# Kernel optimization log

Hardware: AMD Instinct MI355X
Metric: run time of the kernel (lower is better)

Reference implementation:

```python
import jax, jax.numpy as jnp
import numpy as np

ENT_SIZE = 100000; REL_SIZE = 500; ENT_DIM = 256; REL_DIM = 256; H = 256
E = 2048; S = 32; N = 1024; THRESHOLD = 1.0; EPS = 1e-5


def _xav(k, shape):
    fan_in = shape[-1]
    fan_out = shape[-2] if len(shape) > 1 else shape[-1]
    std = (2.0 / (fan_in + fan_out)) ** 0.5
    return jax.random.normal(k, shape, jnp.float32) * std


def setup_inputs() -> dict:
    key = jax.random.key(0)
    ks = jax.random.split(key, 16)
    inp = {}
    inp["neighbors"] = jax.random.randint(ks[0], (E, S), 0, ENT_SIZE)
    inp["pos_h"] = jax.random.randint(ks[1], (N,), 0, E)
    inp["pos_t"] = jax.random.randint(ks[2], (N,), 0, E)
    inp["pos_r"] = jax.random.randint(ks[3], (N,), 0, REL_SIZE)
    inp["neg_h"] = jax.random.randint(ks[4], (N,), 0, E)
    inp["neg_t"] = jax.random.randint(ks[5], (N,), 0, E)
    inp["neg_r"] = jax.random.randint(ks[6], (N,), 0, REL_SIZE)
    inp["ent_embed"] = _xav(ks[7], (ENT_SIZE + 1, ENT_DIM))
    inp["rel_embed"] = _xav(ks[8], (REL_SIZE, REL_DIM))
    inp["trans"] = _xav(ks[9], (2 * REL_SIZE, REL_DIM, ENT_DIM))
    inp["W_ih_f"] = _xav(ks[10], (4 * H, ENT_DIM)); inp["W_hh_f"] = _xav(ks[11], (4 * H, H))
    inp["W_ih_b"] = _xav(ks[12], (4 * H, ENT_DIM)); inp["W_hh_b"] = _xav(ks[13], (4 * H, H))
    inp["b_f"] = jnp.zeros((4 * H,), jnp.float32)
    inp["b_b"] = jnp.zeros((4 * H,), jnp.float32)
    inp["W_lin"] = _xav(ks[14], (ENT_DIM, 2 * H)); inp["b_lin"] = jnp.zeros((ENT_DIM,), jnp.float32)
    inp["gamma"] = jnp.ones((ENT_DIM,), jnp.float32); inp["beta"] = jnp.zeros((ENT_DIM,), jnp.float32)
    return inp


def _lstm_final(x, W_ih, W_hh, b):
    # x: [E,S,D] -> final hidden state [E,H] (PyTorch LSTM gate order i,f,g,o; b = b_ih+b_hh)
    h0 = jnp.zeros((x.shape[0], H), x.dtype)
    def step(carry, xt):
        h, c = carry
        g = xt @ W_ih.T + h @ W_hh.T + b  # [E,4H]
        i, f, gg, o = jnp.split(g, 4, axis=-1)
        c = jax.nn.sigmoid(f) * c + jax.nn.sigmoid(i) * jnp.tanh(gg)
        h = jax.nn.sigmoid(o) * jnp.tanh(c)
        return (h, c), None
    (h, _), _ = jax.lax.scan(step, (h0, h0), jnp.swapaxes(x, 0, 1))
    return h


def _context(ent_embed, neighbors, W_ih_f, W_hh_f, b_f, W_ih_b, W_hh_b, b_b, W_lin, b_lin, gamma, beta):
    x_seq = ent_embed[neighbors]  # [E,S,D]
    h_f = _lstm_final(x_seq, W_ih_f, W_hh_f, b_f)
    h_b = _lstm_final(x_seq[:, ::-1], W_ih_b, W_hh_b, b_b)
    lin = jnp.concatenate([h_f, h_b], -1) @ W_lin.T + b_lin  # [E,ENT_DIM]
    # BatchNorm1d in training mode: batch stats (biased variance)
    mu = lin.mean(0)
    var = lin.var(0)
    return jnp.tanh(gamma * (lin - mu) * jax.lax.rsqrt(var + EPS) + beta)


def _score(trans, rel_embed, ctx, h_idx, r_idx, t_idx):
    Wh = trans[r_idx]             # [N,REL_DIM,ENT_DIM] (grouped expert GEMV, batched)
    Wt = trans[r_idx + REL_SIZE]
    d = jnp.einsum('nre,ne->nr', Wh, ctx[h_idx]) - jnp.einsum('nre,ne->nr', Wt, ctx[t_idx])
    return jnp.linalg.norm(d + rel_embed[r_idx], axis=1)


def reference(neighbors, pos_h, pos_t, pos_r, neg_h, neg_t, neg_r,
              ent_embed, rel_embed, trans, W_ih_f, W_hh_f, W_ih_b, W_hh_b,
              b_f, b_b, W_lin, b_lin, gamma, beta):
    ctx = _context(ent_embed, neighbors, W_ih_f, W_hh_f, b_f, W_ih_b, W_hh_b, b_b,
                   W_lin, b_lin, gamma, beta)
    pos_n = _score(trans, rel_embed, ctx, pos_h, pos_r, pos_t)
    neg_n = _score(trans, rel_embed, ctx, neg_h, neg_r, neg_t)
    return jnp.sum(pos_n + jax.nn.relu(THRESHOLD - neg_n))
```

## Files before the change

### kernel.cpp

```cpp
#include <hip/hip_runtime.h>

constexpr int kE   = 2048;
constexpr int kS   = 32;
constexpr int kD   = 256;
constexpr int kG4  = 1024;
constexpr int kK   = 512;
constexpr int kREL = 500;
constexpr int kN   = 1024;

typedef unsigned short u16;
typedef __attribute__((ext_vector_type(8))) _Float16 f16x8;
typedef __attribute__((ext_vector_type(4))) float    f32x4;

static __device__ __forceinline__ u16 f2h(float f) {
  _Float16 h = (_Float16)f;
  return __builtin_bit_cast(u16, h);
}

__global__ void prep_weights(const float* __restrict__ Wih_f, const float* __restrict__ Whh_f,
                             const float* __restrict__ Wih_b, const float* __restrict__ Whh_b,
                             const float* __restrict__ Wlin_in,
                             u16* __restrict__ Wcat_f, u16* __restrict__ Wcat_b,
                             u16* __restrict__ Wlin) {
  int idx = blockIdx.x * 256 + threadIdx.x;
  if (idx < kG4 * kK) {
    int n = idx >> 9, k = idx & 511;
    float vf = (k < 256) ? Wih_f[n * 256 + k] : Whh_f[n * 256 + (k - 256)];
    float vb = (k < 256) ? Wih_b[n * 256 + k] : Whh_b[n * 256 + (k - 256)];
    Wcat_f[idx] = f2h(vf);
    Wcat_b[idx] = f2h(vb);
  }
  if (idx < 256 * kK) Wlin[idx] = f2h(Wlin_in[idx]);
}

__global__ void gather_x(const int* __restrict__ neighbors, const float* __restrict__ ent,
                         u16* __restrict__ x16) {
  const int tot = kS * kE * kD / 4;
  for (int i = blockIdx.x * blockDim.x + threadIdx.x; i < tot; i += gridDim.x * blockDim.x) {
    int k4 = i & 63;
    int row = i >> 6;
    int e = row & (kE - 1);
    int t = row >> 11;
    int nb = neighbors[e * kS + t];
    float4 v = *(const float4*)(ent + (size_t)nb * kD + k4 * 4);
    ushort4 o;
    o.x = f2h(v.x); o.y = f2h(v.y); o.z = f2h(v.z); o.w = f2h(v.w);
    *(ushort4*)(x16 + (size_t)row * kD + k4 * 4) = o;
  }
}

template <bool GMAP>
static __device__ __forceinline__ void gemm_tile(
    const u16* __restrict__ Alo, const u16* __restrict__ Ahi,
    const u16* __restrict__ W, int e0, int u0,
    u16* As, u16* Bs, f32x4 (&acc)[4][4]) {
  const int tid = threadIdx.x;
  const int lane = tid & 63;
  const int w = tid >> 6;
#pragma unroll
  for (int m = 0; m < 4; m++)
#pragma unroll
    for (int n = 0; n < 4; n++) acc[m][n] = (f32x4){0.f, 0.f, 0.f, 0.f};

  for (int ch = 0; ch < 8; ++ch) {
    const int k0 = ch * 64;
    __syncthreads();
    const u16* Asrc = (k0 < 256) ? Alo : Ahi;
    const int kbase = (k0 < 256) ? k0 : (k0 - 256);
#pragma unroll
    for (int i = 0; i < 2; i++) {
      int idx = tid + i * 256;
      int row = idx >> 3, c8 = idx & 7;
      uint4 v = *(const uint4*)(Asrc + (size_t)(e0 + row) * 256 + kbase + c8 * 8);
      *(uint4*)((char*)As + row * 128 + ((c8 * 16) ^ ((row & 7) << 4))) = v;
    }
#pragma unroll
    for (int i = 0; i < 8; i++) {
      int idx = tid + i * 256;
      int j = idx >> 3, c8 = idx & 7;
      int n = GMAP ? ((j >> 6) * 256 + u0 + (j & 63)) : j;
      uint4 v = *(const uint4*)(W + (size_t)n * kK + k0 + c8 * 8);
      *(uint4*)((char*)Bs + j * 128 + ((c8 * 16) ^ ((j & 7) << 4))) = v;
    }
    __syncthreads();
#pragma unroll
    for (int ks = 0; ks < 2; ++ks) {
      const int kb = ks * 64 + (lane >> 4) * 16;
      f16x8 a[4], b[4];
#pragma unroll
      for (int m = 0; m < 4; m++) {
        int row = m * 16 + (lane & 15);
        a[m] = *(const f16x8*)((const char*)As + row * 128 + (kb ^ ((row & 7) << 4)));
      }
#pragma unroll
      for (int n = 0; n < 4; n++) {
        int row = w * 64 + n * 16 + (lane & 15);
        b[n] = *(const f16x8*)((const char*)Bs + row * 128 + (kb ^ ((row & 7) << 4)));
      }
#pragma unroll
      for (int m = 0; m < 4; m++)
#pragma unroll
        for (int n = 0; n < 4; n++)
          acc[m][n] = __builtin_amdgcn_mfma_f32_16x16x32_f16(a[m], b[n], acc[m][n], 0, 0, 0);
    }
  }
}

__global__ __launch_bounds__(256) void lstm_step(
    const u16* __restrict__ x16, const u16* __restrict__ Wcat_f, const u16* __restrict__ Wcat_b,
    const float* __restrict__ b_f, const float* __restrict__ b_b,
    const u16* __restrict__ hprev, u16* __restrict__ hnext,
    float* __restrict__ cbuf, int t) {
  __shared__ __align__(16) char smem[65536];
  u16* As = (u16*)smem;
  u16* Bs = (u16*)(smem + 8192);
  float* Gs = (float*)smem;

  const int tid = threadIdx.x, lane = tid & 63, w = tid >> 6;
  const int e0 = blockIdx.x * 64, u0 = blockIdx.y * 64, dir = blockIdx.z;

  const u16* Wd = dir ? Wcat_b : Wcat_f;
  const float* bd = dir ? b_b : b_f;
  const u16* xsrc = x16 + (size_t)(dir ? (kS - 1 - t) : t) * kE * kD;
  const u16* hp = hprev + (size_t)dir * kE * kD;
  u16* hn = hnext + (size_t)dir * kE * kD;
  float* cd = cbuf + (size_t)dir * kE * kD;

  f32x4 acc[4][4];
  gemm_tile<true>(xsrc, hp, Wd, e0, u0, As, Bs, acc);

  __syncthreads();
#pragma unroll
  for (int m = 0; m < 4; m++)
#pragma unroll
    for (int n = 0; n < 4; n++)
#pragma unroll
      for (int r = 0; r < 4; r++)
        Gs[(m * 16 + (lane >> 4) * 4 + r) * 256 + w * 64 + n * 16 + (lane & 15)] = acc[m][n][r];
  __syncthreads();

#pragma unroll
  for (int i = 0; i < 16; i++) {
    int cell = tid + i * 256;
    int er = cell >> 6, uu = cell & 63;
    float gi = Gs[er * 256 + uu]        + bd[u0 + uu];
    float gf = Gs[er * 256 + 64 + uu]   + bd[256 + u0 + uu];
    float gg = Gs[er * 256 + 128 + uu]  + bd[512 + u0 + uu];
    float go = Gs[er * 256 + 192 + uu]  + bd[768 + u0 + uu];
    size_t off = (size_t)(e0 + er) * kD + u0 + uu;
    float c_old = cd[off];
    float si = 1.f / (1.f + __expf(-gi));
    float sf = 1.f / (1.f + __expf(-gf));
    float so = 1.f / (1.f + __expf(-go));
    float cn = sf * c_old + si * tanhf(gg);
    cd[off] = cn;
    hn[off] = f2h(so * tanhf(cn));
  }
}

__global__ __launch_bounds__(256) void lin_kernel(
    const u16* __restrict__ hf, const u16* __restrict__ hb,
    const u16* __restrict__ Wl, const float* __restrict__ b_lin,
    float* __restrict__ lin) {
  __shared__ __align__(16) char smem[40960];
  u16* As = (u16*)smem;
  u16* Bs = (u16*)(smem + 8192);
  const int tid = threadIdx.x, lane = tid & 63, w = tid >> 6;
  const int e0 = blockIdx.x * 64;
  f32x4 acc[4][4];
  gemm_tile<false>(hf, hb, Wl, e0, 0, As, Bs, acc);
#pragma unroll
  for (int m = 0; m < 4; m++)
#pragma unroll
    for (int n = 0; n < 4; n++)
#pragma unroll
      for (int r = 0; r < 4; r++) {
        int e = e0 + m * 16 + (lane >> 4) * 4 + r;
        int col = w * 64 + n * 16 + (lane & 15);
        lin[(size_t)e * 256 + col] = acc[m][n][r] + b_lin[col];
      }
}

__global__ void bn_stats(const float* __restrict__ lin, float* __restrict__ part) {
  int b = blockIdx.x, c = threadIdx.x;
  float s = 0.f, s2 = 0.f;
  for (int e = b * 256; e < b * 256 + 256; ++e) {
    float x = lin[(size_t)e * 256 + c];
    s += x; s2 += x * x;
  }
  part[b * 256 + c] = s;
  part[2048 + b * 256 + c] = s2;
}

__global__ void bn_finalize(const float* __restrict__ part, float* __restrict__ mus) {
  int c = threadIdx.x;
  float s = 0.f, s2 = 0.f;
  for (int b = 0; b < 8; b++) { s += part[b * 256 + c]; s2 += part[2048 + b * 256 + c]; }
  float mu = s * (1.f / 2048.f);
  float var = s2 * (1.f / 2048.f) - mu * mu;
  mus[c] = mu;
  mus[256 + c] = rsqrtf(var + 1e-5f);
}

__global__ void bn_tanh(const float* __restrict__ lin, const float* __restrict__ mus,
                        const float* __restrict__ gamma, const float* __restrict__ beta,
                        float* __restrict__ ctx) {
  int idx = blockIdx.x * 256 + threadIdx.x;
  int c = idx & 255;
  float x = lin[idx];
  ctx[idx] = tanhf(gamma[c] * (x - mus[c]) * mus[256 + c] + beta[c]);
}

__global__ __launch_bounds__(256) void score_kernel(
    const float* __restrict__ ctx, const float* __restrict__ trans,
    const float* __restrict__ rel_embed,
    const int* __restrict__ ph, const int* __restrict__ pt, const int* __restrict__ pr,
    const int* __restrict__ nh, const int* __restrict__ nt, const int* __restrict__ nr,
    float* __restrict__ scores) {
  int n = blockIdx.x;
  bool pos = n < kN;
  int m = n & (kN - 1);
  int hi = pos ? ph[m] : nh[m];
  int ti = pos ? pt[m] : nt[m];
  int ri = pos ? pr[m] : nr[m];
  __shared__ float ch[256], ct[256];
  __shared__ float wsum[4];
  int tid = threadIdx.x;
  ch[tid] = ctx[(size_t)hi * 256 + tid];
  ct[tid] = ctx[(size_t)ti * 256 + tid];
  __syncthreads();
  const float4* Wh = (const float4*)(trans + (size_t)ri * 65536 + (size_t)tid * 256);
  const float4* Wt = (const float4*)(trans + ((size_t)ri + kREL) * 65536 + (size_t)tid * 256);
  const float4* c4h = (const float4*)ch;
  const float4* c4t = (const float4*)ct;
  float acc = rel_embed[ri * 256 + tid];
#pragma unroll 4
  for (int q = 0; q < 64; q++) {
    float4 w1 = Wh[q], x1 = c4h[q];
    float4 w2 = Wt[q], x2 = c4t[q];
    acc += w1.x * x1.x + w1.y * x1.y + w1.z * x1.z + w1.w * x1.w;
    acc -= w2.x * x2.x + w2.y * x2.y + w2.z * x2.z + w2.w * x2.w;
  }
  float sq = acc * acc;
  for (int off = 32; off; off >>= 1) sq += __shfl_down(sq, off);
  if ((tid & 63) == 0) wsum[tid >> 6] = sq;
  __syncthreads();
  if (tid == 0) scores[n] = sqrtf(wsum[0] + wsum[1] + wsum[2] + wsum[3]);
}

__global__ void final_reduce(const float* __restrict__ scores, float* __restrict__ out) {
  int tid = threadIdx.x;
  float a = 0.f;
  for (int i = tid; i < 2 * kN; i += 256) {
    float s = scores[i];
    a += (i < kN) ? s : fmaxf(0.f, 1.f - s);
  }
  for (int off = 32; off; off >>= 1) a += __shfl_down(a, off);
  __shared__ float w4[4];
  if ((tid & 63) == 0) w4[tid >> 6] = a;
  __syncthreads();
  if (tid == 0) out[0] = w4[0] + w4[1] + w4[2] + w4[3];
}

extern "C" void kernel_launch(void* const* d_in, const int* in_sizes, int n_in,
                              void* d_out, int out_size, void* d_ws, size_t ws_size,
                              hipStream_t stream) {
  const int*   neighbors = (const int*)d_in[0];
  const int*   pos_h = (const int*)d_in[1];
  const int*   pos_t = (const int*)d_in[2];
  const int*   pos_r = (const int*)d_in[3];
  const int*   neg_h = (const int*)d_in[4];
  const int*   neg_t = (const int*)d_in[5];
  const int*   neg_r = (const int*)d_in[6];
  const float* ent_embed = (const float*)d_in[7];
  const float* rel_embed = (const float*)d_in[8];
  const float* trans = (const float*)d_in[9];
  const float* W_ih_f = (const float*)d_in[10];
  const float* W_hh_f = (const float*)d_in[11];
  const float* W_ih_b = (const float*)d_in[12];
  const float* W_hh_b = (const float*)d_in[13];
  const float* b_f = (const float*)d_in[14];
  const float* b_b = (const float*)d_in[15];
  const float* W_lin = (const float*)d_in[16];
  const float* b_lin = (const float*)d_in[17];
  const float* gamma = (const float*)d_in[18];
  const float* beta = (const float*)d_in[19];

  char* ws = (char*)d_ws;
  size_t off = 0;
  auto alloc = [&](size_t bytes) {
    void* p = ws + off;
    off = (off + bytes + 255) & ~(size_t)255;
    return p;
  };
  u16* Wcat_f = (u16*)alloc((size_t)kG4 * kK * 2);
  u16* Wcat_b = (u16*)alloc((size_t)kG4 * kK * 2);
  u16* Wlin   = (u16*)alloc((size_t)256 * kK * 2);
  u16* x16    = (u16*)alloc((size_t)kS * kE * kD * 2);
  u16* hbuf0  = (u16*)alloc((size_t)2 * kE * kD * 2);
  u16* hbuf1  = (u16*)alloc((size_t)2 * kE * kD * 2);
  float* cbuf = (float*)alloc((size_t)2 * kE * kD * 4);
  float* lin  = (float*)alloc((size_t)kE * 256 * 4);
  float* part = (float*)alloc((size_t)2 * 8 * 256 * 4);
  float* mus  = (float*)alloc((size_t)2 * 256 * 4);
  float* ctx  = (float*)alloc((size_t)kE * 256 * 4);
  float* scores = (float*)alloc((size_t)2 * kN * 4);
  (void)ws_size; (void)in_sizes; (void)n_in; (void)out_size;

  hipMemsetAsync(hbuf0, 0, (size_t)2 * kE * kD * 2, stream);
  hipMemsetAsync(cbuf, 0, (size_t)2 * kE * kD * 4, stream);

  prep_weights<<<2048, 256, 0, stream>>>(W_ih_f, W_hh_f, W_ih_b, W_hh_b, W_lin,
                                         Wcat_f, Wcat_b, Wlin);
  gather_x<<<4096, 256, 0, stream>>>(neighbors, ent_embed, x16);

  for (int t = 0; t < kS; ++t) {
    const u16* hp = (t & 1) ? hbuf1 : hbuf0;
    u16* hn = (t & 1) ? hbuf0 : hbuf1;
    lstm_step<<<dim3(32, 4, 2), 256, 0, stream>>>(x16, Wcat_f, Wcat_b, b_f, b_b, hp, hn, cbuf, t);
  }
  lin_kernel<<<dim3(32, 1), 256, 0, stream>>>(hbuf0, hbuf0 + (size_t)kE * kD, Wlin, b_lin, lin);
  bn_stats<<<8, 256, 0, stream>>>(lin, part);
  bn_finalize<<<1, 256, 0, stream>>>(part, mus);
  bn_tanh<<<2048, 256, 0, stream>>>(lin, mus, gamma, beta, ctx);
  score_kernel<<<2 * kN, 256, 0, stream>>>(ctx, trans, rel_embed,
                                           pos_h, pos_t, pos_r, neg_h, neg_t, neg_r, scores);
  final_reduce<<<1, 256, 0, stream>>>(scores, (float*)d_out);
}
```

Before: 860.2 us.

## Group score GEMVs by relation and use register-direct LSTM step with gate-interleaved weights

Weights are reordered so each wave's 16-column MFMA tiles hold the i,f,g,o gates for the same units. This lets the LSTM step apply the cell update straight from accumulators, with no LDS staging or extra barriers, and operands are loaded directly from global memory. Scoring now buckets triples by relation with a count/scan/scatter pass, so each relation's two 256x256 transform matrices are streamed once per group of up to 8 triples instead of once per triple. This cuts the dominant trans-matrix traffic, at the cost of several small extra kernel launches and load imbalance across relations. Fast exp-based tanh replaces tanhf.

```diff
diff --git a/kernel.cpp b/kernel.cpp
--- a/kernel.cpp
+++ b/kernel.cpp
@@ -16,19 +16,27 @@
   _Float16 h = (_Float16)f;
   return __builtin_bit_cast(u16, h);
 }
+static __device__ __forceinline__ float sigf(float x) { return 1.f / (1.f + __expf(-x)); }
+static __device__ __forceinline__ float tanhfast(float x) {
+  float e = __expf(2.f * x);
+  return 1.f - 2.f / (e + 1.f);
+}
 
 __global__ void prep_weights(const float* __restrict__ Wih_f, const float* __restrict__ Whh_f,
                              const float* __restrict__ Wih_b, const float* __restrict__ Whh_b,
                              const float* __restrict__ Wlin_in,
-                             u16* __restrict__ Wcat_f, u16* __restrict__ Wcat_b,
-                             u16* __restrict__ Wlin) {
+                             u16* __restrict__ Wr, u16* __restrict__ Wlin) {
   int idx = blockIdx.x * 256 + threadIdx.x;
   if (idx < kG4 * kK) {
-    int n = idx >> 9, k = idx & 511;
-    float vf = (k < 256) ? Wih_f[n * 256 + k] : Whh_f[n * 256 + (k - 256)];
-    float vb = (k < 256) ? Wih_b[n * 256 + k] : Whh_b[n * 256 + (k - 256)];
-    Wcat_f[idx] = f2h(vf);
-    Wcat_b[idx] = f2h(vb);
+    int rp = idx >> 9, k = idx & 511;
+    int g = (rp >> 4) & 3;
+    int u = (rp >> 6) * 16 + (rp & 15);
+    int row = g * 256 + u;
+    float vf, vb;
+    if (k < 256) { vf = Wih_f[row * 256 + k];        vb = Wih_b[row * 256 + k]; }
+    else         { vf = Whh_f[row * 256 + k - 256];  vb = Whh_b[row * 256 + k - 256]; }
+    Wr[idx] = f2h(vf);
+    Wr[kG4 * kK + idx] = f2h(vb);
   }
   if (idx < 256 * kK) Wlin[idx] = f2h(Wlin_in[idx]);
 }
@@ -49,6 +57,76 @@
   }
 }
 
+__global__ __launch_bounds__(256) void lstm_step_reg(
+    const u16* __restrict__ x16, const u16* __restrict__ Wr,
+    const float* __restrict__ b_f, const float* __restrict__ b_b,
+    const u16* __restrict__ hprev, u16* __restrict__ hnext,
+    float* __restrict__ cbuf, int t) {
+  const int tid = threadIdx.x, lane = tid & 63, w = tid >> 6;
+  const int bid = blockIdx.x;
+  const int dir = bid >> 7;
+  const int ut  = (bid >> 4) & 7;
+  const int et  = bid & 15;
+  const int wr = w >> 1, wc = w & 1;
+  const int e0 = et * 128 + wr * 64;
+  const int c0 = ut * 128 + wc * 64;
+  const int unit = (c0 >> 6) * 16 + (lane & 15);
+
+  const float* bd = dir ? b_b : b_f;
+  const u16* Wd  = Wr + (size_t)dir * kG4 * kK;
+  const u16* xs  = x16 + (size_t)(dir ? (kS - 1 - t) : t) * kE * kD;
+  const u16* hpd = hprev + (size_t)dir * kE * kD;
+  u16* hnd = hnext + (size_t)dir * kE * kD;
+  float* cd = cbuf + (size_t)dir * kE * kD;
+
+  const int klane = (lane >> 4) * 8;
+
+  f32x4 acc[4][4];
+#pragma unroll
+  for (int m = 0; m < 4; m++)
+#pragma unroll
+    for (int n = 0; n < 4; n++) acc[m][n] = (f32x4){0.f, 0.f, 0.f, 0.f};
+
+#pragma unroll
+  for (int ks = 0; ks < 16; ks++) {
+    const u16* asrc = (ks < 8) ? xs : hpd;
+    const int ka = (ks & 7) * 32 + klane;
+    f16x8 a[4], b[4];
+#pragma unroll
+    for (int m = 0; m < 4; m++) {
+      int row = e0 + m * 16 + (lane & 15);
+      a[m] = *(const f16x8*)(asrc + (size_t)row * kD + ka);
+    }
+#pragma unroll
+    for (int n = 0; n < 4; n++) {
+      int rowp = c0 + n * 16 + (lane & 15);
+      b[n] = *(const f16x8*)(Wd + (size_t)rowp * kK + ks * 32 + klane);
+    }
+#pragma unroll
+    for (int m = 0; m < 4; m++)
+#pragma unroll
+      for (int n = 0; n < 4; n++)
+        acc[m][n] = __builtin_amdgcn_mfma_f32_16x16x32_f16(a[m], b[n], acc[m][n], 0, 0, 0);
+  }
+
+  const float bi = bd[unit], bf_ = bd[256 + unit], bg = bd[512 + unit], bo = bd[768 + unit];
+#pragma unroll
+  for (int m = 0; m < 4; m++)
+#pragma unroll
+    for (int r = 0; r < 4; r++) {
+      int row = e0 + m * 16 + (lane >> 4) * 4 + r;
+      size_t off = (size_t)row * kD + unit;
+      float gi = acc[m][0][r] + bi;
+      float gf = acc[m][1][r] + bf_;
+      float gg = acc[m][2][r] + bg;
+      float go = acc[m][3][r] + bo;
+      float c_old = cd[off];
+      float cn = sigf(gf) * c_old + sigf(gi) * tanhfast(gg);
+      cd[off] = cn;
+      hnd[off] = f2h(sigf(go) * tanhfast(cn));
+    }
+}
+
 template <bool GMAP>
 static __device__ __forceinline__ void gemm_tile(
     const u16* __restrict__ Alo, const u16* __restrict__ Ahi,
@@ -103,58 +181,6 @@
         for (int n = 0; n < 4; n++)
           acc[m][n] = __builtin_amdgcn_mfma_f32_16x16x32_f16(a[m], b[n], acc[m][n], 0, 0, 0);
     }
-  }
-}
-
-__global__ __launch_bounds__(256) void lstm_step(
-    const u16* __restrict__ x16, const u16* __restrict__ Wcat_f, const u16* __restrict__ Wcat_b,
-    const float* __restrict__ b_f, const float* __restrict__ b_b,
-    const u16* __restrict__ hprev, u16* __restrict__ hnext,
-    float* __restrict__ cbuf, int t) {
-  __shared__ __align__(16) char smem[65536];
-  u16* As = (u16*)smem;
-  u16* Bs = (u16*)(smem + 8192);
-  float* Gs = (float*)smem;
-
-  const int tid = threadIdx.x, lane = tid & 63, w = tid >> 6;
-  const int e0 = blockIdx.x * 64, u0 = blockIdx.y * 64, dir = blockIdx.z;
-
-  const u16* Wd = dir ? Wcat_b : Wcat_f;
-  const float* bd = dir ? b_b : b_f;
-  const u16* xsrc = x16 + (size_t)(dir ? (kS - 1 - t) : t) * kE * kD;
-  const u16* hp = hprev + (size_t)dir * kE * kD;
-  u16* hn = hnext + (size_t)dir * kE * kD;
-  float* cd = cbuf + (size_t)dir * kE * kD;
-
-  f32x4 acc[4][4];
-  gemm_tile<true>(xsrc, hp, Wd, e0, u0, As, Bs, acc);
-
-  __syncthreads();
-#pragma unroll
-  for (int m = 0; m < 4; m++)
-#pragma unroll
-    for (int n = 0; n < 4; n++)
-#pragma unroll
-      for (int r = 0; r < 4; r++)
-        Gs[(m * 16 + (lane >> 4) * 4 + r) * 256 + w * 64 + n * 16 + (lane & 15)] = acc[m][n][r];
-  __syncthreads();
-
-#pragma unroll
-  for (int i = 0; i < 16; i++) {
-    int cell = tid + i * 256;
-    int er = cell >> 6, uu = cell & 63;
-    float gi = Gs[er * 256 + uu]        + bd[u0 + uu];
-    float gf = Gs[er * 256 + 64 + uu]   + bd[256 + u0 + uu];
-    float gg = Gs[er * 256 + 128 + uu]  + bd[512 + u0 + uu];
-    float go = Gs[er * 256 + 192 + uu]  + bd[768 + u0 + uu];
-    size_t off = (size_t)(e0 + er) * kD + u0 + uu;
-    float c_old = cd[off];
-    float si = 1.f / (1.f + __expf(-gi));
-    float sf = 1.f / (1.f + __expf(-gf));
-    float so = 1.f / (1.f + __expf(-go));
-    float cn = sf * c_old + si * tanhf(gg);
-    cd[off] = cn;
-    hn[off] = f2h(so * tanhf(cn));
   }
 }
 
@@ -211,41 +237,92 @@
   ctx[idx] = tanhf(gamma[c] * (x - mus[c]) * mus[256 + c] + beta[c]);
 }
 
-__global__ __launch_bounds__(256) void score_kernel(
+__global__ void count_rel(const int* __restrict__ pr, const int* __restrict__ nr,
+                          int* __restrict__ counts) {
+  int i = blockIdx.x * 256 + threadIdx.x;
+  if (i < kN) atomicAdd(&counts[pr[i]], 1);
+  else if (i < 2 * kN) atomicAdd(&counts[nr[i - kN]], 1);
+}
+
+__global__ void scan_rel(const int* __restrict__ counts, int* __restrict__ offs) {
+  __shared__ int s[512];
+  int tid = threadIdx.x;
+  s[tid] = (tid < kREL) ? counts[tid] : 0;
+  __syncthreads();
+  for (int d = 1; d < 512; d <<= 1) {
+    int v = (tid >= d) ? s[tid - d] : 0;
+    __syncthreads();
+    s[tid] += v;
+    __syncthreads();
+  }
+  if (tid == 0) offs[0] = 0;
+  if (tid <= kREL) offs[tid + 1] = s[tid];
+}
+
+__global__ void scatter_rel(const int* __restrict__ pr, const int* __restrict__ nr,
+                            const int* __restrict__ offs, int* __restrict__ cursor,
+                            int* __restrict__ list) {
+  int i = blockIdx.x * 256 + threadIdx.x;
+  if (i >= 2 * kN) return;
+  int r = (i < kN) ? pr[i] : nr[i - kN];
+  int p = atomicAdd(&cursor[r], 1);
+  list[offs[r] + p] = i;
+}
+
+__global__ __launch_bounds__(256) void score_grouped(
     const float* __restrict__ ctx, const float* __restrict__ trans,
     const float* __restrict__ rel_embed,
-    const int* __restrict__ ph, const int* __restrict__ pt, const int* __restrict__ pr,
-    const int* __restrict__ nh, const int* __restrict__ nt, const int* __restrict__ nr,
+    const int* __restrict__ ph, const int* __restrict__ pt,
+    const int* __restrict__ nh, const int* __restrict__ nt,
+    const int* __restrict__ offs, const int* __restrict__ list,
     float* __restrict__ scores) {
-  int n = blockIdx.x;
-  bool pos = n < kN;
-  int m = n & (kN - 1);
-  int hi = pos ? ph[m] : nh[m];
-  int ti = pos ? pt[m] : nt[m];
-  int ri = pos ? pr[m] : nr[m];
-  __shared__ float ch[256], ct[256];
-  __shared__ float wsum[4];
+  int r = blockIdx.x;
+  int start = offs[r], end = offs[r + 1];
+  if (start >= end) return;
   int tid = threadIdx.x;
-  ch[tid] = ctx[(size_t)hi * 256 + tid];
-  ct[tid] = ctx[(size_t)ti * 256 + tid];
-  __syncthreads();
-  const float4* Wh = (const float4*)(trans + (size_t)ri * 65536 + (size_t)tid * 256);
-  const float4* Wt = (const float4*)(trans + ((size_t)ri + kREL) * 65536 + (size_t)tid * 256);
-  const float4* c4h = (const float4*)ch;
-  const float4* c4t = (const float4*)ct;
-  float acc = rel_embed[ri * 256 + tid];
-#pragma unroll 4
-  for (int q = 0; q < 64; q++) {
-    float4 w1 = Wh[q], x1 = c4h[q];
-    float4 w2 = Wt[q], x2 = c4t[q];
-    acc += w1.x * x1.x + w1.y * x1.y + w1.z * x1.z + w1.w * x1.w;
-    acc -= w2.x * x2.x + w2.y * x2.y + w2.z * x2.z + w2.w * x2.w;
-  }
-  float sq = acc * acc;
-  for (int off = 32; off; off >>= 1) sq += __shfl_down(sq, off);
-  if ((tid & 63) == 0) wsum[tid >> 6] = sq;
-  __syncthreads();
-  if (tid == 0) scores[n] = sqrtf(wsum[0] + wsum[1] + wsum[2] + wsum[3]);
+  __shared__ float cs[8][2][256];
+  __shared__ float red[8][4];
+  float relv = rel_embed[r * 256 + tid];
+  const float4* Whp = (const float4*)(trans + (size_t)r * 65536 + (size_t)tid * 256);
+  const float4* Wtp = (const float4*)(trans + ((size_t)r + kREL) * 65536 + (size_t)tid * 256);
+
+  for (int chunk = start; chunk < end; chunk += 8) {
+    int G = min(8, end - chunk);
+    for (int j = 0; j < G; j++) {
+      int i = list[chunk + j];
+      int hh = (i < kN) ? ph[i] : nh[i - kN];
+      int tt = (i < kN) ? pt[i] : nt[i - kN];
+      cs[j][0][tid] = ctx[(size_t)hh * 256 + tid];
+      cs[j][1][tid] = ctx[(size_t)tt * 256 + tid];
+    }
+    __syncthreads();
+    float acc[8];
+#pragma unroll
+    for (int j = 0; j < 8; j++) acc[j] = relv;
+#pragma unroll 2
+    for (int q = 0; q < 64; q++) {
+      float4 w1 = Whp[q];
+      float4 w2 = Wtp[q];
+#pragma unroll
+      for (int j = 0; j < 8; j++) {
+        float4 xh = *(const float4*)&cs[j][0][q * 4];
+        float4 xt = *(const float4*)&cs[j][1][q * 4];
+        acc[j] += w1.x * xh.x + w1.y * xh.y + w1.z * xh.z + w1.w * xh.w
+                - (w2.x * xt.x + w2.y * xt.y + w2.z * xt.z + w2.w * xt.w);
+      }
+    }
+    for (int j = 0; j < G; j++) {
+      float sq = acc[j] * acc[j];
+      for (int o = 32; o; o >>= 1) sq += __shfl_down(sq, o);
+      if ((tid & 63) == 0) red[j][tid >> 6] = sq;
+    }
+    __syncthreads();
+    if (tid < G) {
+      float s = red[tid][0] + red[tid][1] + red[tid][2] + red[tid][3];
+      scores[list[chunk + tid]] = sqrtf(s);
+    }
+    __syncthreads();
+  }
 }
 
 __global__ void final_reduce(const float* __restrict__ scores, float* __restrict__ out) {
@@ -293,37 +370,45 @@
     off = (off + bytes + 255) & ~(size_t)255;
     return p;
   };
-  u16* Wcat_f = (u16*)alloc((size_t)kG4 * kK * 2);
-  u16* Wcat_b = (u16*)alloc((size_t)kG4 * kK * 2);
+  u16* Wr     = (u16*)alloc((size_t)2 * kG4 * kK * 2);
   u16* Wlin   = (u16*)alloc((size_t)256 * kK * 2);
   u16* x16    = (u16*)alloc((size_t)kS * kE * kD * 2);
-  u16* hbuf0  = (u16*)alloc((size_t)2 * kE * kD * 2);
-  u16* hbuf1  = (u16*)alloc((size_t)2 * kE * kD * 2);
+  u16* h0     = (u16*)alloc((size_t)2 * kE * kD * 2);
+  u16* h1     = (u16*)alloc((size_t)2 * kE * kD * 2);
   float* cbuf = (float*)alloc((size_t)2 * kE * kD * 4);
   float* lin  = (float*)alloc((size_t)kE * 256 * 4);
   float* part = (float*)alloc((size_t)2 * 8 * 256 * 4);
   float* mus  = (float*)alloc((size_t)2 * 256 * 4);
   float* ctx  = (float*)alloc((size_t)kE * 256 * 4);
   float* scores = (float*)alloc((size_t)2 * kN * 4);
+  int* zz     = (int*)alloc((size_t)1024 * 4);
+  int* counts = zz;
+  int* cursor = zz + 512;
+  int* offsb  = (int*)alloc((size_t)520 * 4);
+  int* list   = (int*)alloc((size_t)2 * kN * 4);
   (void)ws_size; (void)in_sizes; (void)n_in; (void)out_size;
 
-  hipMemsetAsync(hbuf0, 0, (size_t)2 * kE * kD * 2, stream);
+  hipMemsetAsync(h0, 0, (size_t)2 * kE * kD * 2, stream);
   hipMemsetAsync(cbuf, 0, (size_t)2 * kE * kD * 4, stream);
-
-  prep_weights<<<2048, 256, 0, stream>>>(W_ih_f, W_hh_f, W_ih_b, W_hh_b, W_lin,
-                                         Wcat_f, Wcat_b, Wlin);
+  hipMemsetAsync(zz, 0, (size_t)1024 * 4, stream);
+
+  prep_weights<<<2048, 256, 0, stream>>>(W_ih_f, W_hh_f, W_ih_b, W_hh_b, W_lin, Wr, Wlin);
   gather_x<<<4096, 256, 0, stream>>>(neighbors, ent_embed, x16);
+  count_rel<<<8, 256, 0, stream>>>(pos_r, neg_r, counts);
+  scan_rel<<<1, 512, 0, stream>>>(counts, offsb);
+  scatter_rel<<<8, 256, 0, stream>>>(pos_r, neg_r, offsb, cursor, list);
 
   for (int t = 0; t < kS; ++t) {
-    const u16* hp = (t & 1) ? hbuf1 : hbuf0;
-    u16* hn = (t & 1) ? hbuf0 : hbuf1;
-    lstm_step<<<dim3(32, 4, 2), 256, 0, stream>>>(x16, Wcat_f, Wcat_b, b_f, b_b, hp, hn, cbuf, t);
-  }
-  lin_kernel<<<dim3(32, 1), 256, 0, stream>>>(hbuf0, hbuf0 + (size_t)kE * kD, Wlin, b_lin, lin);
+    const u16* hp = (t & 1) ? h1 : h0;
+    u16* hn = (t & 1) ? h0 : h1;
+    lstm_step_reg<<<256, 256, 0, stream>>>(x16, Wr, b_f, b_b, hp, hn, cbuf, t);
+  }
+
+  lin_kernel<<<dim3(32, 1), 256, 0, stream>>>(h0, h0 + (size_t)kE * kD, Wlin, b_lin, lin);
   bn_stats<<<8, 256, 0, stream>>>(lin, part);
   bn_finalize<<<1, 256, 0, stream>>>(part, mus);
   bn_tanh<<<2048, 256, 0, stream>>>(lin, mus, gamma, beta, ctx);
-  score_kernel<<<2 * kN, 256, 0, stream>>>(ctx, trans, rel_embed,
-                                           pos_h, pos_t, pos_r, neg_h, neg_t, neg_r, scores);
+  score_grouped<<<kREL, 256, 0, stream>>>(ctx, trans, rel_embed,
+                                          pos_h, pos_t, neg_h, neg_t, offsb, list, scores);
   final_reduce<<<1, 256, 0, stream>>>(scores, (float*)d_out);
 }
```

Result: no change. 858.1 us (-0.2%).
